# Optimization experiments

Hardware: AMD Instinct MI355X
Metric: run time of the kernel (lower is better)

## Reference

```python
import jax, jax.numpy as jnp
import numpy as np

VOXEL_SIZE = jnp.array([0.1, 0.1, 0.2], jnp.float32)
PC_RANGE = jnp.array([-51.2, -51.2, -5.0, 51.2, 51.2, 3.0], jnp.float32)
GRID = (1024, 1024, 40)
MAX_POINTS = 10
MAX_VOXELS = 120000


def setup_inputs() -> dict:
    key = jax.random.key(0)
    N, C = 1_200_000, 5
    u = jax.random.uniform(key, (N, C), dtype=jnp.float32)
    # map xyz into (slightly beyond) the point-cloud range so some points fall outside,
    # exercising the validity masking; features 3,4 stay in [0,1)
    lo = jnp.array([-53.0, -53.0, -5.5, 0.0, 0.0], jnp.float32)
    hi = jnp.array([53.0, 53.0, 3.5, 1.0, 1.0], jnp.float32)
    points = lo + u * (hi - lo)
    return {"points": points}


def _voxelize(points):
    """Hard voxelization. Returns fixed-size buffers (padded to MAX_VOXELS)
    plus voxel_num; buffer[:voxel_num] equals the torch module's output."""
    N, C = points.shape
    gx, gy, gz = GRID
    grid = jnp.array(GRID, jnp.int32)

    # per-point voxel coordinate (cx, cy, cz) and validity
    coor = jnp.floor((points[:, :3] - PC_RANGE[:3]) / VOXEL_SIZE).astype(jnp.int32)
    valid = jnp.all((coor >= 0) & (coor < grid), axis=1)

    # linearized voxel id; invalid points routed to a sentinel that sorts last
    lin = coor[:, 0] * (gy * gz) + coor[:, 1] * gz + coor[:, 2]
    SENTINEL = gx * gy * gz
    lin = jnp.where(valid, lin, SENTINEL)

    # stable sort groups points of the same voxel; within a group original
    # point indices are increasing (matches the serial visit order)
    order = jnp.argsort(lin, stable=True)
    lin_s = lin[order]
    valid_s = valid[order]

    # run (group) starts in sorted order
    starts = jnp.concatenate([valid_s[:1], (lin_s[1:] != lin_s[:-1]) & valid_s[1:]])
    run_id = jnp.maximum(jnp.cumsum(starts.astype(jnp.int32)) - 1, 0)
    ar = jnp.arange(N, dtype=jnp.int32)

    # slot within voxel = position within run
    first_sorted_pos = jax.ops.segment_min(ar, run_id, num_segments=N)
    pos_in_run = ar - first_sorted_pos[run_id]

    # voxel index = visit-order rank of the first point of each group
    first_orig = jax.ops.segment_min(order.astype(jnp.int32), run_id, num_segments=N)
    is_first = jnp.zeros((N,), bool).at[order].set(starts)
    rank = jnp.cumsum(is_first.astype(jnp.int32)) - 1  # in original point order
    vidx_s = rank[first_orig[run_id]]

    # scatter points into voxel buffer (caps on voxels and points-per-voxel)
    write = valid_s & (vidx_s < MAX_VOXELS) & (pos_in_run < MAX_POINTS)
    vi = jnp.where(write, vidx_s, MAX_VOXELS)  # out-of-range -> dropped
    si = jnp.where(write, pos_in_run, 0)
    voxels = jnp.zeros((MAX_VOXELS, MAX_POINTS, C), points.dtype)
    voxels = voxels.at[vi, si].set(points[order], mode='drop')

    # voxel coordinates (cx, cy, cz), one write per created voxel
    cw = starts & (vidx_s < MAX_VOXELS)
    ci = jnp.where(cw, vidx_s, MAX_VOXELS)
    coors = jnp.zeros((MAX_VOXELS, 3), jnp.int32).at[ci].set(coor[order], mode='drop')

    num_points_per_voxel = jax.ops.segment_sum(
        write.astype(jnp.int32), vi, num_segments=MAX_VOXELS + 1)[:MAX_VOXELS]

    voxel_num = jnp.minimum(jnp.sum(is_first.astype(jnp.int32)), MAX_VOXELS)
    return voxels, coors, num_points_per_voxel, voxel_num


def reference(points):
    return _voxelize(points)
```

## Files before the change

### kernel.cpp

```cpp
#include <hip/hip_runtime.h>
#include <stdint.h>


#define GXD 1024
#define GYD 1024
#define GZD 40
#define GYZ (GYD * GZD)
#define MAXV 120000
#define MAXP 10
#define CAP 16

#define HBITS 22
#define HSIZE (1u << HBITS)
#define HMASK (HSIZE - 1u)
#define KEYMASK ((1ull << 26) - 1ull)
#define EMPTY64 0xFFFFFFFFFFFFFFFFull

__device__ __forceinline__ unsigned hash_lin(unsigned l) {
    return (l * 2654435761u) >> (32 - HBITS);
}

__global__ void k1_assign(const float* __restrict__ pts, int n,
                          int* __restrict__ lin_arr, int* __restrict__ slot_arr,
                          unsigned long long* __restrict__ table) {
    int i = blockIdx.x * blockDim.x + threadIdx.x;
    if (i >= n) return;
    float x = pts[(size_t)i * 5 + 0];
    float y = pts[(size_t)i * 5 + 1];
    float z = pts[(size_t)i * 5 + 2];
    int cx = (int)floorf((x - (-51.2f)) / 0.1f);
    int cy = (int)floorf((y - (-51.2f)) / 0.1f);
    int cz = (int)floorf((z - (-5.0f)) / 0.2f);
    bool valid = (cx >= 0) & (cx < GXD) & (cy >= 0) & (cy < GYD) & (cz >= 0) & (cz < GZD);
    if (!valid) { lin_arr[i] = -1; slot_arr[i] = -1; return; }
    unsigned l = (unsigned)(cx * GYZ + cy * GZD + cz);
    lin_arr[i] = (int)l;
    unsigned long long want = ((unsigned long long)(unsigned)i << 26) | (unsigned long long)l;
    unsigned s = hash_lin(l);
    while (true) {
        unsigned long long cur = table[s];
        if (cur == EMPTY64) {
            unsigned long long prev = atomicCAS(&table[s], EMPTY64, want);
            if (prev == EMPTY64) break;
            cur = prev;
        }
        if ((cur & KEYMASK) == (unsigned long long)l) {
            if ((cur >> 26) > (unsigned long long)(unsigned)i)
                atomicMin(&table[s], want);
            break;
        }
        s = (s + 1) & HMASK;
    }
    slot_arr[i] = (int)s;
}

__global__ void k2a_mark(int n, const int* __restrict__ slot_arr,
                         const unsigned long long* __restrict__ table,
                         unsigned long long* __restrict__ flagWords,
                         int* __restrict__ blockCnt) {
    int i = blockIdx.x * blockDim.x + threadIdx.x;
    bool first = false;
    if (i < n) {
        int s = slot_arr[i];
        if (s >= 0) {
            unsigned long long v = table[s];
            first = ((v >> 26) == (unsigned long long)(unsigned)i);
        }
    }
    unsigned long long m = __ballot(first);
    __shared__ int ws[4];
    int lane = threadIdx.x & 63, w = threadIdx.x >> 6;
    if (lane == 0) { flagWords[(size_t)blockIdx.x * 4 + w] = m; ws[w] = __popcll(m); }
    __syncthreads();
    if (threadIdx.x == 0)
        blockCnt[blockIdx.x] = ws[0] + ws[1] + ws[2] + ws[3];
}

__global__ void k2b_scan(int nb, const int* __restrict__ blockCnt,
                         int* __restrict__ blockOff,
                         float* __restrict__ voxel_num_out) {
    __shared__ int tsum[256];
    __shared__ int toff[256];
    int t = threadIdx.x;
    int chunk = (nb + 255) / 256;
    int lo = t * chunk;
    int hi = lo + chunk; if (hi > nb) hi = nb;
    int s = 0;
    for (int j = lo; j < hi; ++j) s += blockCnt[j];
    tsum[t] = s;
    __syncthreads();
    if (t == 0) {
        int acc = 0;
        for (int j = 0; j < 256; ++j) { int v = tsum[j]; toff[j] = acc; acc += v; }
        int vn = acc < MAXV ? acc : MAXV;
        *voxel_num_out = (float)vn;
    }
    __syncthreads();
    int off = toff[t];
    for (int j = lo; j < hi; ++j) { blockOff[j] = off; off += blockCnt[j]; }
}

__global__ void k2c_rank(int n, const int* __restrict__ lin_arr,
                         const int* __restrict__ slot_arr,
                         const unsigned long long* __restrict__ flagWords,
                         const int* __restrict__ blockOff,
                         unsigned long long* __restrict__ table,
                         float* __restrict__ coors_out) {
    int i = blockIdx.x * blockDim.x + threadIdx.x;
    int lane = threadIdx.x & 63, w = threadIdx.x >> 6;
    unsigned long long m = flagWords[(size_t)blockIdx.x * 4 + w];
    __shared__ int ws[4];
    if (lane == 0) ws[w] = __popcll(m);
    __syncthreads();
    bool first = (i < n) && ((m >> lane) & 1ull);
    if (!first) return;
    int off = blockOff[blockIdx.x];
    for (int j = 0; j < w; ++j) off += ws[j];
    int rank = off + (int)__popcll(m & ((1ull << lane) - 1ull));
    if (rank >= MAXV) return;
    int l = lin_arr[i];
    int s = slot_arr[i];
    table[s] = (1ull << 63) | ((unsigned long long)(unsigned)rank << 26)
             | (unsigned long long)(unsigned)l;
    int cx = l / GYZ;
    int r = l - cx * GYZ;
    int cy = r / GZD;
    int cz = r - cy * GZD;
    coors_out[(size_t)rank * 3 + 0] = (float)cx;
    coors_out[(size_t)rank * 3 + 1] = (float)cy;
    coors_out[(size_t)rank * 3 + 2] = (float)cz;
}

__global__ void k3_append(int n, const int* __restrict__ slot_arr,
                          const unsigned long long* __restrict__ table,
                          int* __restrict__ vcount, int* __restrict__ vlist) {
    int i = blockIdx.x * blockDim.x + threadIdx.x;
    if (i >= n) return;
    int s = slot_arr[i];
    if (s < 0) return;
    unsigned long long v = table[s];
    if (!(v >> 63)) return;
    int rank = (int)((v >> 26) & 0x1FFFFFull);
    int pos = atomicAdd(&vcount[rank], 1);
    if (pos < CAP) vlist[(size_t)rank * CAP + pos] = i;
}

__global__ void k4_emit(const float* __restrict__ pts,
                        const int* __restrict__ vcount,
                        const int* __restrict__ vlist,
                        float* __restrict__ vox_out, float* __restrict__ num_out,
                        int* __restrict__ ovflCnt, int* __restrict__ ovflList) {
    int v = blockIdx.x * blockDim.x + threadIdx.x;
    if (v >= MAXV) return;
    int cnt = vcount[v];
    if (cnt == 0) return;
    if (cnt > CAP) {
        int e = atomicAdd(ovflCnt, 1);
        if (e < 1024) ovflList[e] = v;
        return;
    }
    int idx[CAP];
    for (int j = 0; j < cnt; ++j) idx[j] = vlist[(size_t)v * CAP + j];
    for (int a = 1; a < cnt; ++a) {
        int key = idx[a];
        int b = a - 1;
        while (b >= 0 && idx[b] > key) { idx[b + 1] = idx[b]; --b; }
        idx[b + 1] = key;
    }
    int np = cnt < MAXP ? cnt : MAXP;
    num_out[v] = (float)np;
    for (int s = 0; s < np; ++s) {
        const float* p = pts + (size_t)idx[s] * 5;
        float* o = vox_out + ((size_t)v * MAXP + s) * 5;
        o[0] = p[0]; o[1] = p[1]; o[2] = p[2]; o[3] = p[3]; o[4] = p[4];
    }
}

__global__ void k5_ovfl(const float* __restrict__ pts, int n,
                        const int* __restrict__ lin_arr,
                        const int* __restrict__ vcount,
                        const int* __restrict__ ovflCnt,
                        const int* __restrict__ ovflList,
                        const float* __restrict__ coors_out,
                        float* __restrict__ vox_out, float* __restrict__ num_out) {
    if (threadIdx.x != 0 || blockIdx.x != 0) return;
    int cnt = *ovflCnt;
    if (cnt > 1024) cnt = 1024;
    for (int e = 0; e < cnt; ++e) {
        int v = ovflList[e];
        int cx = (int)coors_out[(size_t)v * 3 + 0];
        int cy = (int)coors_out[(size_t)v * 3 + 1];
        int cz = (int)coors_out[(size_t)v * 3 + 2];
        int target = cx * GYZ + cy * GZD + cz;
        int found = 0;
        for (int i = 0; i < n && found < MAXP; ++i) {
            if (lin_arr[i] == target) {
                const float* p = pts + (size_t)i * 5;
                float* o = vox_out + ((size_t)v * MAXP + found) * 5;
                for (int c = 0; c < 5; ++c) o[c] = p[c];
                ++found;
            }
        }
        int np = vcount[v] < MAXP ? vcount[v] : MAXP;
        num_out[v] = (float)np;
    }
}

extern "C" void kernel_launch(void* const* d_in, const int* in_sizes, int n_in,
                              void* d_out, int out_size, void* d_ws, size_t ws_size,
                              hipStream_t stream) {
    const float* pts = (const float*)d_in[0];
    int n = in_sizes[0] / 5;
    int nb = (n + 255) / 256;

    float* out = (float*)d_out;
    float* vox_out   = out;
    float* coors_out = out + 6000000;
    float* num_out   = out + 6360000;
    float* vn_out    = out + 6480000;

    char* w = (char*)d_ws;
    unsigned long long* table = (unsigned long long*)w;  w += (size_t)HSIZE * 8;
    int* lin_arr   = (int*)w;               w += (size_t)n * 4;
    int* slot_arr  = (int*)w;               w += (size_t)n * 4;
    int* blockCnt  = (int*)w;               w += (size_t)nb * 4;
    int* blockOff  = (int*)w;               w += (size_t)nb * 4;
    unsigned long long* flagWords = (unsigned long long*)w; w += (size_t)nb * 4 * 8;
    int* vlist     = (int*)w;               w += (size_t)MAXV * CAP * 4;
    int* vcount    = (int*)w;               w += (size_t)MAXV * 4;
    int* ovflCnt   = (int*)w;               w += 4;
    int* ovflList  = (int*)w;               w += 1024 * 4;

    hipMemsetAsync(d_out, 0, (size_t)out_size * 4, stream);
    hipMemsetAsync(table, 0xFF, (size_t)HSIZE * 8, stream);
    hipMemsetAsync(vcount, 0, ((size_t)MAXV + 1) * 4, stream);

    k1_assign<<<nb, 256, 0, stream>>>(pts, n, lin_arr, slot_arr, table);
    k2a_mark<<<nb, 256, 0, stream>>>(n, slot_arr, table, flagWords, blockCnt);
    k2b_scan<<<1, 256, 0, stream>>>(nb, blockCnt, blockOff, vn_out);
    k2c_rank<<<nb, 256, 0, stream>>>(n, lin_arr, slot_arr, flagWords, blockOff,
                                     table, coors_out);
    k3_append<<<nb, 256, 0, stream>>>(n, slot_arr, table, vcount, vlist);
    k4_emit<<<(MAXV + 255) / 256, 256, 0, stream>>>(pts, vcount, vlist, vox_out,
                                                    num_out, ovflCnt, ovflList);
    k5_ovfl<<<1, 64, 0, stream>>>(pts, n, lin_arr, vcount, ovflCnt, ovflList,
                                  coors_out, vox_out, num_out);
}
```

Baseline: 197.1 us.

## Build first-point flag mask by sweeping hash table instead of per-point check

Replaces the per-point first-occurrence check, which did a random table lookup for every point, with a sweep over the hash table that sets a bit per winning point index via atomicOr. The scan now derives per-block counts from the mask words. Ranks go into a per-point rankOf array instead of being written back into table entries, and k3 reads rankOf through the stored minimum index. Probing also now issues atomicCAS directly without a plain load first. The sweep reads the whole 32MB table and adds atomics, and k3 gains an extra dependent gather.

```diff
diff --git a/kernel.cpp b/kernel.cpp
--- a/kernel.cpp
+++ b/kernel.cpp
@@ -38,12 +38,8 @@
     unsigned long long want = ((unsigned long long)(unsigned)i << 26) | (unsigned long long)l;
     unsigned s = hash_lin(l);
     while (true) {
-        unsigned long long cur = table[s];
-        if (cur == EMPTY64) {
-            unsigned long long prev = atomicCAS(&table[s], EMPTY64, want);
-            if (prev == EMPTY64) break;
-            cur = prev;
-        }
+        unsigned long long cur = atomicCAS(&table[s], EMPTY64, want);
+        if (cur == EMPTY64) break;
         if ((cur & KEYMASK) == (unsigned long long)l) {
             if ((cur >> 26) > (unsigned long long)(unsigned)i)
                 atomicMin(&table[s], want);
@@ -54,29 +50,17 @@
     slot_arr[i] = (int)s;
 }
 
-__global__ void k2a_mark(int n, const int* __restrict__ slot_arr,
-                         const unsigned long long* __restrict__ table,
-                         unsigned long long* __restrict__ flagWords,
-                         int* __restrict__ blockCnt) {
-    int i = blockIdx.x * blockDim.x + threadIdx.x;
-    bool first = false;
-    if (i < n) {
-        int s = slot_arr[i];
-        if (s >= 0) {
-            unsigned long long v = table[s];
-            first = ((v >> 26) == (unsigned long long)(unsigned)i);
-        }
-    }
-    unsigned long long m = __ballot(first);
-    __shared__ int ws[4];
-    int lane = threadIdx.x & 63, w = threadIdx.x >> 6;
-    if (lane == 0) { flagWords[(size_t)blockIdx.x * 4 + w] = m; ws[w] = __popcll(m); }
-    __syncthreads();
-    if (threadIdx.x == 0)
-        blockCnt[blockIdx.x] = ws[0] + ws[1] + ws[2] + ws[3];
-}
-
-__global__ void k2b_scan(int nb, const int* __restrict__ blockCnt,
+__global__ void k2s_sweep(const unsigned long long* __restrict__ table,
+                          unsigned long long* __restrict__ flagMask) {
+    unsigned s = blockIdx.x * blockDim.x + threadIdx.x;
+    if (s >= HSIZE) return;
+    unsigned long long v = table[s];
+    if (v == EMPTY64) return;
+    unsigned m = (unsigned)(v >> 26);
+    atomicOr(&flagMask[m >> 6], 1ull << (m & 63));
+}
+
+__global__ void k2b_scan(int nb, const unsigned long long* __restrict__ flagMask,
                          int* __restrict__ blockOff,
                          float* __restrict__ voxel_num_out) {
     __shared__ int tsum[256];
@@ -86,7 +70,10 @@
     int lo = t * chunk;
     int hi = lo + chunk; if (hi > nb) hi = nb;
     int s = 0;
-    for (int j = lo; j < hi; ++j) s += blockCnt[j];
+    for (int j = lo; j < hi; ++j) {
+        const unsigned long long* wds = &flagMask[(size_t)j * 4];
+        s += __popcll(wds[0]) + __popcll(wds[1]) + __popcll(wds[2]) + __popcll(wds[3]);
+    }
     tsum[t] = s;
     __syncthreads();
     if (t == 0) {
@@ -97,18 +84,21 @@
     }
     __syncthreads();
     int off = toff[t];
-    for (int j = lo; j < hi; ++j) { blockOff[j] = off; off += blockCnt[j]; }
+    for (int j = lo; j < hi; ++j) {
+        blockOff[j] = off;
+        const unsigned long long* wds = &flagMask[(size_t)j * 4];
+        off += __popcll(wds[0]) + __popcll(wds[1]) + __popcll(wds[2]) + __popcll(wds[3]);
+    }
 }
 
 __global__ void k2c_rank(int n, const int* __restrict__ lin_arr,
-                         const int* __restrict__ slot_arr,
-                         const unsigned long long* __restrict__ flagWords,
+                         const unsigned long long* __restrict__ flagMask,
                          const int* __restrict__ blockOff,
-                         unsigned long long* __restrict__ table,
+                         int* __restrict__ rankOf,
                          float* __restrict__ coors_out) {
     int i = blockIdx.x * blockDim.x + threadIdx.x;
     int lane = threadIdx.x & 63, w = threadIdx.x >> 6;
-    unsigned long long m = flagWords[(size_t)blockIdx.x * 4 + w];
+    unsigned long long m = flagMask[(size_t)blockIdx.x * 4 + w];
     __shared__ int ws[4];
     if (lane == 0) ws[w] = __popcll(m);
     __syncthreads();
@@ -117,11 +107,9 @@
     int off = blockOff[blockIdx.x];
     for (int j = 0; j < w; ++j) off += ws[j];
     int rank = off + (int)__popcll(m & ((1ull << lane) - 1ull));
+    rankOf[i] = rank;
     if (rank >= MAXV) return;
     int l = lin_arr[i];
-    int s = slot_arr[i];
-    table[s] = (1ull << 63) | ((unsigned long long)(unsigned)rank << 26)
-             | (unsigned long long)(unsigned)l;
     int cx = l / GYZ;
     int r = l - cx * GYZ;
     int cy = r / GZD;
@@ -133,14 +121,16 @@
 
 __global__ void k3_append(int n, const int* __restrict__ slot_arr,
                           const unsigned long long* __restrict__ table,
+                          const int* __restrict__ rankOf,
                           int* __restrict__ vcount, int* __restrict__ vlist) {
     int i = blockIdx.x * blockDim.x + threadIdx.x;
     if (i >= n) return;
     int s = slot_arr[i];
     if (s < 0) return;
     unsigned long long v = table[s];
-    if (!(v >> 63)) return;
-    int rank = (int)((v >> 26) & 0x1FFFFFull);
+    int m = (int)(v >> 26);
+    int rank = rankOf[m];
+    if (rank >= MAXV) return;
     int pos = atomicAdd(&vcount[rank], 1);
     if (pos < CAP) vlist[(size_t)rank * CAP + pos] = i;
 }
@@ -223,24 +213,25 @@
     unsigned long long* table = (unsigned long long*)w;  w += (size_t)HSIZE * 8;
     int* lin_arr   = (int*)w;               w += (size_t)n * 4;
     int* slot_arr  = (int*)w;               w += (size_t)n * 4;
-    int* blockCnt  = (int*)w;               w += (size_t)nb * 4;
+    int* rankOf    = (int*)w;               w += (size_t)n * 4;
     int* blockOff  = (int*)w;               w += (size_t)nb * 4;
-    unsigned long long* flagWords = (unsigned long long*)w; w += (size_t)nb * 4 * 8;
     int* vlist     = (int*)w;               w += (size_t)MAXV * CAP * 4;
+    unsigned long long* flagMask = (unsigned long long*)w; w += (size_t)nb * 4 * 8;
     int* vcount    = (int*)w;               w += (size_t)MAXV * 4;
     int* ovflCnt   = (int*)w;               w += 4;
     int* ovflList  = (int*)w;               w += 1024 * 4;
+    size_t zeroBytes = (size_t)nb * 4 * 8 + (size_t)MAXV * 4 + 4;
 
     hipMemsetAsync(d_out, 0, (size_t)out_size * 4, stream);
     hipMemsetAsync(table, 0xFF, (size_t)HSIZE * 8, stream);
-    hipMemsetAsync(vcount, 0, ((size_t)MAXV + 1) * 4, stream);
+    hipMemsetAsync(flagMask, 0, zeroBytes, stream);
 
     k1_assign<<<nb, 256, 0, stream>>>(pts, n, lin_arr, slot_arr, table);
-    k2a_mark<<<nb, 256, 0, stream>>>(n, slot_arr, table, flagWords, blockCnt);
-    k2b_scan<<<1, 256, 0, stream>>>(nb, blockCnt, blockOff, vn_out);
-    k2c_rank<<<nb, 256, 0, stream>>>(n, lin_arr, slot_arr, flagWords, blockOff,
-                                     table, coors_out);
-    k3_append<<<nb, 256, 0, stream>>>(n, slot_arr, table, vcount, vlist);
+    k2s_sweep<<<HSIZE / 256, 256, 0, stream>>>(table, flagMask);
+    k2b_scan<<<1, 256, 0, stream>>>(nb, flagMask, blockOff, vn_out);
+    k2c_rank<<<nb, 256, 0, stream>>>(n, lin_arr, flagMask, blockOff, rankOf,
+                                     coors_out);
+    k3_append<<<nb, 256, 0, stream>>>(n, slot_arr, table, rankOf, vcount, vlist);
     k4_emit<<<(MAXV + 255) / 256, 256, 0, stream>>>(pts, vcount, vlist, vox_out,
                                                     num_out, ovflCnt, ovflList);
     k5_ovfl<<<1, 64, 0, stream>>>(pts, n, lin_arr, vcount, ovflCnt, ovflList,
```

Result: slower. 227.2 us (+15.3%).
